# Performance work log

Measured on AMD Instinct MI355X. Metric: run time of the kernel, lower is better.

Reference implementation:

```python
import jax, jax.numpy as jnp
import numpy as np

N = 50000
E = 640000
F_IN = 128
F_OUT = 128


def setup_inputs() -> dict:
    key = jax.random.key(0)
    k1, k2, k3, k4, k5 = jax.random.split(key, 5)
    x = jax.random.normal(k1, (N, F_IN), dtype=jnp.float32)
    edge_index = jax.random.randint(k2, (2, E), 0, N, dtype=jnp.int64)
    s = 1.0 / np.sqrt(F_IN)
    W_l = jax.random.uniform(k3, (F_IN, F_OUT), minval=-s, maxval=s, dtype=jnp.float32)
    W_r = jax.random.uniform(k4, (F_IN, F_OUT), minval=-s, maxval=s, dtype=jnp.float32)
    b = jax.random.uniform(k5, (F_OUT,), minval=-s, maxval=s, dtype=jnp.float32)
    return {"x": x, "edge_index": edge_index, "W_l": W_l, "W_r": W_r, "b": b}


def reference(x, edge_index, W_l, W_r, b):
    src, dst = edge_index[0], edge_index[1]
    # gather source-node features along edges: [E, F_in]
    msgs = x[src]
    # mean aggregation at destination nodes
    summed = jax.ops.segment_sum(msgs, dst, num_segments=N)          # [N, F_in]
    counts = jax.ops.segment_sum(jnp.ones((E,), jnp.float32), dst, num_segments=N)
    mean_nb = summed / jnp.maximum(counts, 1.0)[:, None]
    # SAGEConv: lin_l(aggregated) + lin_r(self), bias on lin_l only
    out = mean_nb @ W_l + x @ W_r + b
    return jax.nn.relu(out)
```

## Files before the change

### kernel.cpp

```cpp
#include <hip/hip_runtime.h>

#define N_NODES 50000
#define E_EDGES 640000
#define F 128

typedef __attribute__((ext_vector_type(8))) short short8;
typedef __attribute__((ext_vector_type(4))) float f32x4;

#define DEG_OFF 0
#define OFF_OFF 200704
#define CUR_OFF 401408
#define BSUM_OFF 601600
#define BPRE_OFF 602624
#define WF_OFF 603648
#define SRC_OFF 734720

__device__ __forceinline__ unsigned short f2bf(float f) {
    unsigned int u = __builtin_bit_cast(unsigned int, f);
    u += 0x7FFFu + ((u >> 16) & 1u);
    return (unsigned short)(u >> 16);
}

__global__ __launch_bounds__(256) void gnn_hist(const int* __restrict__ ei,
                                                int* __restrict__ deg) {
    const int i = blockIdx.x * blockDim.x + threadIdx.x;
    const int stride = gridDim.x * blockDim.x;
    for (int e = i; e < E_EDGES; e += stride)
        atomicAdd(&deg[ei[E_EDGES + e]], 1);
}

__global__ __launch_bounds__(256) void gnn_scan_a(const int* __restrict__ deg,
                                                  int* __restrict__ off,
                                                  int* __restrict__ bsum) {
    __shared__ int s[256];
    const int t = threadIdx.x;
    const int i = blockIdx.x * 256 + t;
    const int v = (i < N_NODES) ? deg[i] : 0;
    s[t] = v;
    __syncthreads();
    for (int d = 1; d < 256; d <<= 1) {
        const int u = (t >= d) ? s[t - d] : 0;
        __syncthreads();
        s[t] += u;
        __syncthreads();
    }
    if (i < N_NODES) off[i] = s[t] - v;
    if (t == 255) bsum[blockIdx.x] = s[255];
}

__global__ __launch_bounds__(256) void gnn_scan_b(const int* __restrict__ bsum,
                                                  int* __restrict__ bpre,
                                                  int* __restrict__ off) {
    __shared__ int s[256];
    const int t = threadIdx.x;
    const int v = (t < 196) ? bsum[t] : 0;
    s[t] = v;
    __syncthreads();
    for (int d = 1; d < 256; d <<= 1) {
        const int u = (t >= d) ? s[t - d] : 0;
        __syncthreads();
        s[t] += u;
        __syncthreads();
    }
    if (t < 196) bpre[t] = s[t] - v;
    if (t == 255) off[N_NODES] = s[255];
}

__global__ __launch_bounds__(256) void gnn_scan_c(const int* __restrict__ bpre,
                                                  int* __restrict__ off,
                                                  int* __restrict__ cur) {
    const int i = blockIdx.x * 256 + threadIdx.x;
    if (i < N_NODES) {
        const int o = off[i] + bpre[blockIdx.x];
        off[i] = o;
        cur[i] = o;
    }
}

__global__ __launch_bounds__(256) void gnn_fill(const int* __restrict__ ei,
                                                int* __restrict__ cur,
                                                int* __restrict__ srcs) {
    const int i = blockIdx.x * blockDim.x + threadIdx.x;
    const int stride = gridDim.x * blockDim.x;
    for (int e = i; e < E_EDGES; e += stride) {
        const int d = ei[E_EDGES + e];
        const int p = atomicAdd(&cur[d], 1);
        srcs[p] = ei[e];
    }
}

__global__ __launch_bounds__(256) void gnn_wprep(const float* __restrict__ Wl,
                                                 const float* __restrict__ Wr,
                                                 short* __restrict__ Wf) {
    const int tid = blockIdx.x * 256 + threadIdx.x;
    const int lane = tid & 63;
    const int frag = tid >> 6;
    const int kstep = frag >> 3;
    const int ct = frag & 7;
    const int kb = kstep * 32 + (lane >> 4) * 8;
    const int c = ct * 16 + (lane & 15);
    short8 v;
#pragma unroll
    for (int j = 0; j < 8; ++j) {
        const int k = kb + j;
        const float f = (k < F) ? Wl[k * F + c] : Wr[(k - F) * F + c];
        v[j] = (short)f2bf(f);
    }
    *reinterpret_cast<short8*>(Wf + (size_t)tid * 8) = v;
}

__global__ __launch_bounds__(256) void gnn_aggregate(
    const float* __restrict__ x, const int* __restrict__ off,
    const int* __restrict__ srcs, float* __restrict__ out) {
    const int node = blockIdx.x * 4 + (threadIdx.x >> 6);
    if (node >= N_NODES) return;
    const int lane = threadIdx.x & 63;
    const int half = lane >> 5;
    const int l32 = lane & 31;
    const int o0 = off[node];
    const int o1 = off[node + 1];
    f32x4 acc0 = {0.f, 0.f, 0.f, 0.f};
    f32x4 acc1 = {0.f, 0.f, 0.f, 0.f};
    int j = o0;
    for (; j + 4 <= o1; j += 4) {
        const int sA = srcs[j + half];
        const int sB = srcs[j + 2 + half];
        acc0 += *reinterpret_cast<const f32x4*>(x + (size_t)sA * F + l32 * 4);
        acc1 += *reinterpret_cast<const f32x4*>(x + (size_t)sB * F + l32 * 4);
    }
    for (; j < o1; j += 2) {
        const int jj = j + half;
        const int s = srcs[(jj < o1) ? jj : o0];
        f32x4 v = *reinterpret_cast<const f32x4*>(x + (size_t)s * F + l32 * 4);
        if (jj >= o1) v = (f32x4){0.f, 0.f, 0.f, 0.f};
        acc0 += v;
    }
    acc0 += acc1;
    f32x4 o;
    o[0] = __shfl_xor(acc0[0], 32, 64);
    o[1] = __shfl_xor(acc0[1], 32, 64);
    o[2] = __shfl_xor(acc0[2], 32, 64);
    o[3] = __shfl_xor(acc0[3], 32, 64);
    acc0 += o;
    if (half == 0) {
        const float inv = 1.0f / (float)max(o1 - o0, 1);
        acc0 *= inv;
        *reinterpret_cast<f32x4*>(out + (size_t)node * F + l32 * 4) = acc0;
    }
}

__global__ __launch_bounds__(256) void gnn_finalize_mfma(
    const float* __restrict__ x, const short* __restrict__ Wf,
    const float* __restrict__ bias, float* __restrict__ out) {
    const int t = threadIdx.x;
    const int lane = t & 63;
    const int wv = t >> 6;
    const int r0 = blockIdx.x * 64 + wv * 16;
    const int rl = lane & 15;
    const int kg = lane >> 4;
    const int arow = r0 + rl;
    const int arow_c = (arow < N_NODES) ? arow : (N_NODES - 1);

    f32x4 acc[8];
#pragma unroll
    for (int ct = 0; ct < 8; ++ct) acc[ct] = (f32x4){0.f, 0.f, 0.f, 0.f};

#pragma unroll
    for (int kstep = 0; kstep < 8; ++kstep) {
        const int k0 = kstep * 32 + kg * 8;
        const float* asrc = (kstep < 4) ? (out + (size_t)arow_c * F + k0)
                                        : (x + (size_t)arow_c * F + (k0 - F));
        const float4 a0 = *reinterpret_cast<const float4*>(asrc);
        const float4 a1 = *reinterpret_cast<const float4*>(asrc + 4);
        short8 af;
        af[0] = (short)f2bf(a0.x);
        af[1] = (short)f2bf(a0.y);
        af[2] = (short)f2bf(a0.z);
        af[3] = (short)f2bf(a0.w);
        af[4] = (short)f2bf(a1.x);
        af[5] = (short)f2bf(a1.y);
        af[6] = (short)f2bf(a1.z);
        af[7] = (short)f2bf(a1.w);
#pragma unroll
        for (int ct = 0; ct < 8; ++ct) {
            const short8 bf = *reinterpret_cast<const short8*>(
                Wf + (size_t)((kstep * 8 + ct) * 64 + lane) * 8);
            acc[ct] = __builtin_amdgcn_mfma_f32_16x16x32_bf16(af, bf, acc[ct],
                                                              0, 0, 0);
        }
    }

#pragma unroll
    for (int ct = 0; ct < 8; ++ct) {
        const int c = ct * 16 + rl;
        const float bv = bias[c];
#pragma unroll
        for (int r = 0; r < 4; ++r) {
            const int row = r0 + kg * 4 + r;
            if (row < N_NODES)
                out[(size_t)row * F + c] = fmaxf(acc[ct][r] + bv, 0.0f);
        }
    }
}

extern "C" void kernel_launch(void* const* d_in, const int* in_sizes, int n_in,
                              void* d_out, int out_size, void* d_ws,
                              size_t ws_size, hipStream_t stream) {
    const float* x = (const float*)d_in[0];
    const int* ei = (const int*)d_in[1];
    const float* Wl = (const float*)d_in[2];
    const float* Wr = (const float*)d_in[3];
    const float* b = (const float*)d_in[4];
    float* out = (float*)d_out;

    char* ws = (char*)d_ws;
    int* deg = (int*)(ws + DEG_OFF);
    int* off = (int*)(ws + OFF_OFF);
    int* cur = (int*)(ws + CUR_OFF);
    int* bsum = (int*)(ws + BSUM_OFF);
    int* bpre = (int*)(ws + BPRE_OFF);
    short* Wf = (short*)(ws + WF_OFF);
    int* srcs = (int*)(ws + SRC_OFF);

    hipMemsetAsync(deg, 0, N_NODES * sizeof(int), stream);

    gnn_hist<<<2048, 256, 0, stream>>>(ei, deg);
    gnn_scan_a<<<196, 256, 0, stream>>>(deg, off, bsum);
    gnn_scan_b<<<1, 256, 0, stream>>>(bsum, bpre, off);
    gnn_scan_c<<<196, 256, 0, stream>>>(bpre, off, cur);
    gnn_fill<<<2048, 256, 0, stream>>>(ei, cur, srcs);
    gnn_wprep<<<16, 256, 0, stream>>>(Wl, Wr, Wf);
    gnn_aggregate<<<(N_NODES + 3) / 4, 256, 0, stream>>>(x, off, srcs, out);
    gnn_finalize_mfma<<<(N_NODES + 63) / 64, 256, 0, stream>>>(x, Wf, b, out);
}
```

Baseline: 221.0 us.

## Pre-cast node features to bf16 and aggregate from bf16 gather

Adds a pass that converts x to bf16 once. The edge gather-and-mean then reads half-width rows with more accumulators in flight and writes the mean as bf16. The MFMA finalize reads bf16 operands directly instead of converting fp32 in the inner loop. This roughly halves the bytes moved by the random gather, which likely dominates, at the cost of an extra cast pass over x, lower-precision accumulation inputs, and a dependence on a larger workspace (it falls back otherwise).

```diff
diff --git a/kernel.cpp b/kernel.cpp
--- a/kernel.cpp
+++ b/kernel.cpp
@@ -14,11 +14,17 @@
 #define BPRE_OFF 602624
 #define WF_OFF 603648
 #define SRC_OFF 734720
+#define XBF_OFF 3294720
+#define MBF_OFF 16094720
+#define WS_NEED_FULL 28894720ULL
 
 __device__ __forceinline__ unsigned short f2bf(float f) {
     unsigned int u = __builtin_bit_cast(unsigned int, f);
     u += 0x7FFFu + ((u >> 16) & 1u);
     return (unsigned short)(u >> 16);
+}
+__device__ __forceinline__ float bfhi2f(unsigned int hi16) {
+    return __builtin_bit_cast(float, hi16 & 0xFFFF0000u);
 }
 
 __global__ __launch_bounds__(256) void gnn_hist(const int* __restrict__ ei,
@@ -107,6 +113,128 @@
         v[j] = (short)f2bf(f);
     }
     *reinterpret_cast<short8*>(Wf + (size_t)tid * 8) = v;
+}
+
+__global__ __launch_bounds__(256) void gnn_xcast(const float* __restrict__ x,
+                                                 unsigned short* __restrict__ xbf) {
+    const size_t i = ((size_t)blockIdx.x * 256 + threadIdx.x) * 8;
+    if (i >= (size_t)N_NODES * F) return;
+    const float4 a0 = *reinterpret_cast<const float4*>(x + i);
+    const float4 a1 = *reinterpret_cast<const float4*>(x + i + 4);
+    short8 v;
+    v[0] = (short)f2bf(a0.x); v[1] = (short)f2bf(a0.y);
+    v[2] = (short)f2bf(a0.z); v[3] = (short)f2bf(a0.w);
+    v[4] = (short)f2bf(a1.x); v[5] = (short)f2bf(a1.y);
+    v[6] = (short)f2bf(a1.z); v[7] = (short)f2bf(a1.w);
+    *reinterpret_cast<short8*>((short*)xbf + i) = v;
+}
+
+__global__ __launch_bounds__(256) void gnn_aggregate_bf(
+    const unsigned short* __restrict__ xbf, const int* __restrict__ off,
+    const int* __restrict__ srcs, unsigned short* __restrict__ mbf) {
+    const int node = blockIdx.x * 4 + (threadIdx.x >> 6);
+    if (node >= N_NODES) return;
+    const int lane = threadIdx.x & 63;
+    const int half = lane >> 5;
+    const int l32 = lane & 31;
+    const int o0 = off[node];
+    const int o1 = off[node + 1];
+    const unsigned short* xb = xbf + (size_t)l32 * 4;
+    f32x4 acc0 = {0.f, 0.f, 0.f, 0.f}, acc1 = {0.f, 0.f, 0.f, 0.f};
+    f32x4 acc2 = {0.f, 0.f, 0.f, 0.f}, acc3 = {0.f, 0.f, 0.f, 0.f};
+    int j = o0;
+    for (; j + 8 <= o1; j += 8) {
+        const uint2 a = *reinterpret_cast<const uint2*>(xb + (size_t)srcs[j + half] * F);
+        const uint2 b = *reinterpret_cast<const uint2*>(xb + (size_t)srcs[j + 2 + half] * F);
+        const uint2 c = *reinterpret_cast<const uint2*>(xb + (size_t)srcs[j + 4 + half] * F);
+        const uint2 d = *reinterpret_cast<const uint2*>(xb + (size_t)srcs[j + 6 + half] * F);
+        acc0[0] += bfhi2f(a.x << 16); acc0[1] += bfhi2f(a.x);
+        acc0[2] += bfhi2f(a.y << 16); acc0[3] += bfhi2f(a.y);
+        acc1[0] += bfhi2f(b.x << 16); acc1[1] += bfhi2f(b.x);
+        acc1[2] += bfhi2f(b.y << 16); acc1[3] += bfhi2f(b.y);
+        acc2[0] += bfhi2f(c.x << 16); acc2[1] += bfhi2f(c.x);
+        acc2[2] += bfhi2f(c.y << 16); acc2[3] += bfhi2f(c.y);
+        acc3[0] += bfhi2f(d.x << 16); acc3[1] += bfhi2f(d.x);
+        acc3[2] += bfhi2f(d.y << 16); acc3[3] += bfhi2f(d.y);
+    }
+    for (; j + 4 <= o1; j += 4) {
+        const uint2 a = *reinterpret_cast<const uint2*>(xb + (size_t)srcs[j + half] * F);
+        const uint2 b = *reinterpret_cast<const uint2*>(xb + (size_t)srcs[j + 2 + half] * F);
+        acc0[0] += bfhi2f(a.x << 16); acc0[1] += bfhi2f(a.x);
+        acc0[2] += bfhi2f(a.y << 16); acc0[3] += bfhi2f(a.y);
+        acc1[0] += bfhi2f(b.x << 16); acc1[1] += bfhi2f(b.x);
+        acc1[2] += bfhi2f(b.y << 16); acc1[3] += bfhi2f(b.y);
+    }
+    for (; j < o1; j += 2) {
+        const int jj = j + half;
+        const uint2 a = *reinterpret_cast<const uint2*>(
+            xb + (size_t)srcs[(jj < o1) ? jj : o0] * F);
+        if (jj < o1) {
+            acc0[0] += bfhi2f(a.x << 16); acc0[1] += bfhi2f(a.x);
+            acc0[2] += bfhi2f(a.y << 16); acc0[3] += bfhi2f(a.y);
+        }
+    }
+    acc0 += acc1 + acc2 + acc3;
+    f32x4 o;
+    o[0] = __shfl_xor(acc0[0], 32, 64);
+    o[1] = __shfl_xor(acc0[1], 32, 64);
+    o[2] = __shfl_xor(acc0[2], 32, 64);
+    o[3] = __shfl_xor(acc0[3], 32, 64);
+    acc0 += o;
+    if (half == 0) {
+        const float inv = 1.0f / (float)max(o1 - o0, 1);
+        acc0 *= inv;
+        ushort4 m;
+        m.x = f2bf(acc0[0]); m.y = f2bf(acc0[1]);
+        m.z = f2bf(acc0[2]); m.w = f2bf(acc0[3]);
+        *reinterpret_cast<ushort4*>(mbf + (size_t)node * F + l32 * 4) = m;
+    }
+}
+
+__global__ __launch_bounds__(256) void gnn_finalize_bf(
+    const unsigned short* __restrict__ xbf, const unsigned short* __restrict__ mbf,
+    const short* __restrict__ Wf, const float* __restrict__ bias,
+    float* __restrict__ out) {
+    const int t = threadIdx.x;
+    const int lane = t & 63;
+    const int wv = t >> 6;
+    const int r0 = blockIdx.x * 64 + wv * 16;
+    const int rl = lane & 15;
+    const int kg = lane >> 4;
+    const int arow = r0 + rl;
+    const int arow_c = (arow < N_NODES) ? arow : (N_NODES - 1);
+
+    f32x4 acc[8];
+#pragma unroll
+    for (int ct = 0; ct < 8; ++ct) acc[ct] = (f32x4){0.f, 0.f, 0.f, 0.f};
+
+#pragma unroll
+    for (int kstep = 0; kstep < 8; ++kstep) {
+        const int k0 = kstep * 32 + kg * 8;
+        const unsigned short* asrc =
+            (kstep < 4) ? (mbf + (size_t)arow_c * F + k0)
+                        : (xbf + (size_t)arow_c * F + (k0 - F));
+        const short8 af = *reinterpret_cast<const short8*>(asrc);
+#pragma unroll
+        for (int ct = 0; ct < 8; ++ct) {
+            const short8 bf = *reinterpret_cast<const short8*>(
+                Wf + (size_t)((kstep * 8 + ct) * 64 + lane) * 8);
+            acc[ct] = __builtin_amdgcn_mfma_f32_16x16x32_bf16(af, bf, acc[ct],
+                                                              0, 0, 0);
+        }
+    }
+
+#pragma unroll
+    for (int ct = 0; ct < 8; ++ct) {
+        const int c = ct * 16 + rl;
+        const float bv = bias[c];
+#pragma unroll
+        for (int r = 0; r < 4; ++r) {
+            const int row = r0 + kg * 4 + r;
+            if (row < N_NODES)
+                out[(size_t)row * F + c] = fmaxf(acc[ct][r] + bv, 0.0f);
+        }
+    }
 }
 
 __global__ __launch_bounds__(256) void gnn_aggregate(
@@ -160,11 +288,9 @@
     const int kg = lane >> 4;
     const int arow = r0 + rl;
     const int arow_c = (arow < N_NODES) ? arow : (N_NODES - 1);
-
     f32x4 acc[8];
 #pragma unroll
     for (int ct = 0; ct < 8; ++ct) acc[ct] = (f32x4){0.f, 0.f, 0.f, 0.f};
-
 #pragma unroll
     for (int kstep = 0; kstep < 8; ++kstep) {
         const int k0 = kstep * 32 + kg * 8;
@@ -173,14 +299,10 @@
         const float4 a0 = *reinterpret_cast<const float4*>(asrc);
         const float4 a1 = *reinterpret_cast<const float4*>(asrc + 4);
         short8 af;
-        af[0] = (short)f2bf(a0.x);
-        af[1] = (short)f2bf(a0.y);
-        af[2] = (short)f2bf(a0.z);
-        af[3] = (short)f2bf(a0.w);
-        af[4] = (short)f2bf(a1.x);
-        af[5] = (short)f2bf(a1.y);
-        af[6] = (short)f2bf(a1.z);
-        af[7] = (short)f2bf(a1.w);
+        af[0] = (short)f2bf(a0.x); af[1] = (short)f2bf(a0.y);
+        af[2] = (short)f2bf(a0.z); af[3] = (short)f2bf(a0.w);
+        af[4] = (short)f2bf(a1.x); af[5] = (short)f2bf(a1.y);
+        af[6] = (short)f2bf(a1.z); af[7] = (short)f2bf(a1.w);
 #pragma unroll
         for (int ct = 0; ct < 8; ++ct) {
             const short8 bf = *reinterpret_cast<const short8*>(
@@ -189,7 +311,6 @@
                                                               0, 0, 0);
         }
     }
-
 #pragma unroll
     for (int ct = 0; ct < 8; ++ct) {
         const int c = ct * 16 + rl;
@@ -221,6 +342,8 @@
     int* bpre = (int*)(ws + BPRE_OFF);
     short* Wf = (short*)(ws + WF_OFF);
     int* srcs = (int*)(ws + SRC_OFF);
+    unsigned short* xbf = (unsigned short*)(ws + XBF_OFF);
+    unsigned short* mbf = (unsigned short*)(ws + MBF_OFF);
 
     hipMemsetAsync(deg, 0, N_NODES * sizeof(int), stream);
 
@@ -230,6 +353,16 @@
     gnn_scan_c<<<196, 256, 0, stream>>>(bpre, off, cur);
     gnn_fill<<<2048, 256, 0, stream>>>(ei, cur, srcs);
     gnn_wprep<<<16, 256, 0, stream>>>(Wl, Wr, Wf);
-    gnn_aggregate<<<(N_NODES + 3) / 4, 256, 0, stream>>>(x, off, srcs, out);
-    gnn_finalize_mfma<<<(N_NODES + 63) / 64, 256, 0, stream>>>(x, Wf, b, out);
-}
+
+    if (ws_size >= WS_NEED_FULL) {
+        gnn_xcast<<<((N_NODES * F / 8) + 255) / 256, 256, 0, stream>>>(x, xbf);
+        gnn_aggregate_bf<<<(N_NODES + 3) / 4, 256, 0, stream>>>(xbf, off, srcs,
+                                                                mbf);
+        gnn_finalize_bf<<<(N_NODES + 63) / 64, 256, 0, stream>>>(xbf, mbf, Wf,
+                                                                 b, out);
+    } else {
+        gnn_aggregate<<<(N_NODES + 3) / 4, 256, 0, stream>>>(x, off, srcs, out);
+        gnn_finalize_mfma<<<(N_NODES + 63) / 64, 256, 0, stream>>>(x, Wf, b,
+                                                                   out);
+    }
+}
```

Measured after the change: 202.1 us. -8.6%, faster.
